# Kernel optimization log

Measured on AMD Instinct MI355X. Metric: run time of the kernel, lower is better.

## Reference

```python
import jax, jax.numpy as jnp
import numpy as np

D_MODEL = 1024
N_HEADS = 16
D_K = D_MODEL // N_HEADS
BATCH = 4
SEQ = 2048


def setup_inputs() -> dict:
    key = jax.random.key(0)
    ks = jax.random.split(key, 12)
    s = 1.0 / np.sqrt(D_MODEL)
    inp = {
        "query": jax.random.normal(ks[0], (BATCH, SEQ, D_MODEL), jnp.float32),
        "key": jax.random.normal(ks[1], (BATCH, SEQ, D_MODEL), jnp.float32),
        "value": jax.random.normal(ks[2], (BATCH, SEQ, D_MODEL), jnp.float32),
        # causal mask: True = masked (ignored), broadcastable over batch/heads
        "mask": jnp.triu(jnp.ones((SEQ, SEQ), bool), k=1)[None, None, :, :],
        "w_q": jax.random.normal(ks[3], (D_MODEL, D_MODEL), jnp.float32) * s,
        "b_q": jax.random.normal(ks[4], (D_MODEL,), jnp.float32) * s,
        "w_k": jax.random.normal(ks[5], (D_MODEL, D_MODEL), jnp.float32) * s,
        "b_k": jax.random.normal(ks[6], (D_MODEL,), jnp.float32) * s,
        "w_v": jax.random.normal(ks[7], (D_MODEL, D_MODEL), jnp.float32) * s,
        "b_v": jax.random.normal(ks[8], (D_MODEL,), jnp.float32) * s,
        "w_o": jax.random.normal(ks[9], (D_MODEL, D_MODEL), jnp.float32) * s,
        "b_o": jax.random.normal(ks[10], (D_MODEL,), jnp.float32) * s,
    }
    return inp


def _split_heads(x):
    # (B, S, D) -> (B, H, S, d_k)
    b, s, _ = x.shape
    return x.reshape(b, s, N_HEADS, D_K).transpose(0, 2, 1, 3)


def reference(query, key, value, mask, w_q, b_q, w_k, b_k, w_v, b_v, w_o, b_o):
    # torch Linear: y = x @ W.T + b
    q = _split_heads(query @ w_q.T + b_q)
    k = _split_heads(key @ w_k.T + b_k)
    v = _split_heads(value @ w_v.T + b_v)
    scale = 1.0 / jnp.sqrt(jnp.asarray(D_K, q.dtype))
    scores = jnp.einsum("bhqd,bhkd->bhqk", q, k) * scale
    scores = jnp.where(mask, jnp.asarray(-jnp.inf, scores.dtype), scores)
    weights = jax.nn.softmax(scores, axis=-1)  # dropout p=0.0 (eval)
    attn = jnp.einsum("bhqk,bhkd->bhqd", weights, v)
    b = attn.shape[0]
    attn = attn.transpose(0, 2, 1, 3).reshape(b, -1, D_MODEL)
    return attn @ w_o.T + b_o
```

## Files before the change

kernel.cpp:

```cpp
#include <hip/hip_runtime.h>

#define S_LEN 2048
#define DMODEL 1024
#define H_CNT 16
#define DK 64
#define BATCH 4

typedef __attribute__((ext_vector_type(8))) short short8;
typedef __attribute__((ext_vector_type(4))) float f32x4;
typedef __attribute__((ext_vector_type(16))) float f32x16;

static __device__ __forceinline__ short f2bf(float f) {
  union { float f; unsigned u; } x; x.f = f;
  unsigned r = x.u + 0x7fffu + ((x.u >> 16) & 1u);
  return (short)(r >> 16);
}

static __device__ __forceinline__ unsigned cvt_pk_bf16(float lo, float hi) {
  unsigned r;
  asm("v_cvt_pk_bf16_f32 %0, %1, %2" : "=v"(r) : "v"(lo), "v"(hi));
  return r;
}

static __device__ __forceinline__ void gl_lds16(const short* g, short* l) {
  __builtin_amdgcn_global_load_lds((const __attribute__((address_space(1))) void*)g,
                                   (__attribute__((address_space(3))) void*)l, 16, 0, 0);
}

__global__ __launch_bounds__(256) void cast_kernel(const float* __restrict__ src,
                                                   short* __restrict__ dst, int n8) {
  int i = blockIdx.x * 256 + threadIdx.x;
  if (i >= n8) return;
  const float4* s4 = (const float4*)src;
  float4 a = s4[2 * i], b = s4[2 * i + 1];
  short8 o;
  o[0] = f2bf(a.x); o[1] = f2bf(a.y); o[2] = f2bf(a.z); o[3] = f2bf(a.w);
  o[4] = f2bf(b.x); o[5] = f2bf(b.y); o[6] = f2bf(b.z); o[7] = f2bf(b.w);
  ((short8*)dst)[i] = o;
}

template <int MODE>
__global__ __launch_bounds__(256) void gemm_bt(const short* __restrict__ A,
                                               const short* __restrict__ B,
                                               const float* __restrict__ bias,
                                               void* __restrict__ Cout,
                                               int M, int N, int K, float scl) {
  __shared__ short Sab[(128 + 64) * 32];
  const int tid = threadIdx.x;
  const int lane = tid & 63, wid = tid >> 6;
  const int lin = blockIdx.x;
  const int w = (lin & 7) * 128 + (lin >> 3);
  int bx, by;
  if (MODE == 1) { bx = w >> 3; by = w & 7; }
  else           { bx = w & 15; by = w >> 4; }
  const int m0 = by * 128, n0 = bx * 64;
  const int wr = wid * 32;
  const int lrow = lane & 15, lk8 = (lane >> 4) * 8;

  const int l4 = lane >> 2, lc = (lane & 3) * 8;
  const short* gsrc[3];
  short* ldst[3];
#pragma unroll
  for (int i = 0; i < 3; i++) {
    int c = wid * 3 + i;
    ldst[i] = &Sab[c * 512];
    if (c < 8) gsrc[i] = &A[(size_t)(m0 + c * 16 + l4) * K + lc];
    else       gsrc[i] = &B[(size_t)(n0 + (c - 8) * 16 + l4) * K + lc];
  }

  f32x4 acc[2][4] = {};

  for (int k0 = 0; k0 < K; k0 += 32) {
#pragma unroll
    for (int i = 0; i < 3; i++) gl_lds16(gsrc[i] + k0, ldst[i]);
    __syncthreads();
    short8 af[2], bfr[4];
#pragma unroll
    for (int m = 0; m < 2; m++) af[m] = *(const short8*)(&Sab[(wr + m * 16 + lrow) * 32 + lk8]);
#pragma unroll
    for (int n = 0; n < 4; n++) bfr[n] = *(const short8*)(&Sab[(128 + n * 16 + lrow) * 32 + lk8]);
#pragma unroll
    for (int m = 0; m < 2; m++)
#pragma unroll
      for (int n = 0; n < 4; n++)
        acc[m][n] = __builtin_amdgcn_mfma_f32_16x16x32_bf16(af[m], bfr[n], acc[m][n], 0, 0, 0);
    __syncthreads();
  }

  const int g4 = (lane >> 4) * 4;
#pragma unroll
  for (int n = 0; n < 4; n++) {
    const int col = n0 + n * 16 + lrow;
#pragma unroll
    for (int m = 0; m < 2; m++) {
#pragma unroll
      for (int i = 0; i < 4; i++) {
        const int row = m0 + wr + m * 16 + g4 + i;
        float val = acc[m][n][i];
        if (MODE == 0) {
          val = (val + bias[col]) * scl;
          int b = row >> 11, s2 = row & 2047, h = col >> 6, d = col & 63;
          ((short*)Cout)[((size_t)(b * H_CNT + h) * S_LEN + s2) * DK + d] = f2bf(val);
        } else if (MODE == 1) {
          val = val + bias[row];
          int h = row >> 6, d = row & 63, b = col >> 11, s2 = col & 2047;
          ((short*)Cout)[((size_t)(b * H_CNT + h) * DK + d) * S_LEN + s2] = f2bf(val);
        } else {
          val = val + bias[col];
          ((float*)Cout)[(size_t)row * N + col] = val;
        }
      }
    }
  }
}

__global__ __launch_bounds__(256, 4) void attn2_kernel(const short* __restrict__ Q,
                                                       const short* __restrict__ Kc,
                                                       const short* __restrict__ Vt,
                                                       short* __restrict__ Oout) {
  const int bh = blockIdx.y;
  const int j = blockIdx.x;
  const int wid = threadIdx.x >> 6, lane = threadIdx.x & 63;
  const int qt = (wid == 0) ? j : (wid == 1) ? (31 - j) : (wid == 2) ? (32 + j) : (63 - j);
  const int q0 = qt * 32;
  const int ql = lane & 31, hl = lane >> 5;

  const short* Qb = Q + (size_t)bh * S_LEN * DK;
  const short* Kb = Kc + (size_t)bh * S_LEN * DK;
  const short* Vb = Vt + (size_t)bh * DK * S_LEN;

  short8 qf[4];
#pragma unroll
  for (int kk = 0; kk < 4; kk++)
    qf[kk] = *(const short8*)(&Qb[(q0 + ql) * DK + kk * 16 + hl * 8]);

  f32x16 oacc[2] = {};
  float mr = -1e30f, lr = 0.f;

  const int ntiles = qt + 1;
  for (int t = 0; t < ntiles; t++) {
    const int kv0 = t * 32;
    f32x16 st = {};
#pragma unroll
    for (int kk = 0; kk < 4; kk++) {
      short8 kf = *(const short8*)(&Kb[(kv0 + ql) * DK + kk * 16 + hl * 8]);
      st = __builtin_amdgcn_mfma_f32_32x32x16_bf16(kf, qf[kk], st, 0, 0, 0);
    }
    short8 vf[2][2];
#pragma unroll
    for (int td = 0; td < 2; td++)
#pragma unroll
      for (int kk = 0; kk < 2; kk++)
        vf[td][kk] = *(const short8*)(&Vb[(size_t)(td * 32 + ql) * S_LEN + kv0 + kk * 16 + hl * 8]);

    float p[16];
#pragma unroll
    for (int r = 0; r < 16; r++) p[r] = st[r];
    if (t == ntiles - 1) {
#pragma unroll
      for (int r = 0; r < 16; r++) {
        int kvr = (r & 3) + 8 * (r >> 2) + 4 * hl;
        if (kvr > ql) p[r] = -1e30f;
      }
    }
    float pm = p[0];
#pragma unroll
    for (int r = 1; r < 16; r++) pm = fmaxf(pm, p[r]);
    pm = fmaxf(pm, __shfl_xor(pm, 32, 64));
    if (!__all(pm <= mr + 8.f)) {
      float mnew = fmaxf(mr, pm);
      float al = __builtin_amdgcn_exp2f(mr - mnew);
      lr *= al;
#pragma unroll
      for (int td = 0; td < 2; td++)
#pragma unroll
        for (int r = 0; r < 16; r++) oacc[td][r] *= al;
      mr = mnew;
    }
    float rs = 0.f;
#pragma unroll
    for (int r = 0; r < 16; r++) {
      p[r] = __builtin_amdgcn_exp2f(p[r] - mr);
      rs += p[r];
    }
    rs += __shfl_xor(rs, 32, 64);
    lr += rs;

    unsigned wpk[8];
#pragma unroll
    for (int tt = 0; tt < 8; tt++) wpk[tt] = cvt_pk_bf16(p[2 * tt], p[2 * tt + 1]);
    union { short8 s; unsigned u[4]; } bf0, bf1;
    {
      unsigned xa = __shfl_xor((int)wpk[2], 32, 64), xb = __shfl_xor((int)wpk[0], 32, 64);
      bf0.u[0] = hl ? xa : wpk[0];
      bf0.u[2] = hl ? wpk[2] : xb;
    }
    {
      unsigned xa = __shfl_xor((int)wpk[3], 32, 64), xb = __shfl_xor((int)wpk[1], 32, 64);
      bf0.u[1] = hl ? xa : wpk[1];
      bf0.u[3] = hl ? wpk[3] : xb;
    }
    {
      unsigned xa = __shfl_xor((int)wpk[6], 32, 64), xb = __shfl_xor((int)wpk[4], 32, 64);
      bf1.u[0] = hl ? xa : wpk[4];
      bf1.u[2] = hl ? wpk[6] : xb;
    }
    {
      unsigned xa = __shfl_xor((int)wpk[7], 32, 64), xb = __shfl_xor((int)wpk[5], 32, 64);
      bf1.u[1] = hl ? xa : wpk[5];
      bf1.u[3] = hl ? wpk[7] : xb;
    }

#pragma unroll
    for (int td = 0; td < 2; td++) {
      oacc[td] = __builtin_amdgcn_mfma_f32_32x32x16_bf16(vf[td][0], bf0.s, oacc[td], 0, 0, 0);
      oacc[td] = __builtin_amdgcn_mfma_f32_32x32x16_bf16(vf[td][1], bf1.s, oacc[td], 0, 0, 0);
    }
  }

  const float inv = __builtin_amdgcn_rcpf(lr);
  const int b = bh >> 4, h = bh & 15;
  unsigned* ob = (unsigned*)Oout + ((size_t)b * S_LEN + q0 + ql) * (DMODEL / 2) + h * (DK / 2);
#pragma unroll
  for (int td = 0; td < 2; td++)
#pragma unroll
    for (int tt = 0; tt < 8; tt++) {
      unsigned pkv = cvt_pk_bf16(oacc[td][2 * tt] * inv, oacc[td][2 * tt + 1] * inv);
      ob[td * 16 + (tt & 1) + 4 * (tt >> 1) + 2 * hl] = pkv;
    }
}

extern "C" void kernel_launch(void* const* d_in, const int* in_sizes, int n_in,
                              void* d_out, int out_size, void* d_ws, size_t ws_size,
                              hipStream_t stream) {
  (void)in_sizes; (void)n_in; (void)out_size; (void)ws_size;
  const float* query = (const float*)d_in[0];
  const float* key_i = (const float*)d_in[1];
  const float* value = (const float*)d_in[2];
  const float* w_q = (const float*)d_in[4];
  const float* b_q = (const float*)d_in[5];
  const float* w_k = (const float*)d_in[6];
  const float* b_k = (const float*)d_in[7];
  const float* w_v = (const float*)d_in[8];
  const float* b_v = (const float*)d_in[9];
  const float* w_o = (const float*)d_in[10];
  const float* b_o = (const float*)d_in[11];

  const size_t XE = (size_t)BATCH * S_LEN * DMODEL;
  const size_t WE = (size_t)DMODEL * DMODEL;

  short* xq = (short*)d_ws;
  short* xk = xq + XE;
  short* xv = xk + XE;
  short* wq = xv + XE;
  short* wk = wq + WE;
  short* wv = wk + WE;
  short* wo = wv + WE;
  short* qb = wo + WE;
  short* kb = qb + XE;
  short* vtb = kb + XE;
  short* attnb = xq;

  const int M = BATCH * S_LEN;

  int n8x = (int)(XE / 8), n8w = (int)(WE / 8);
  cast_kernel<<<dim3((n8x + 255) / 256), 256, 0, stream>>>(query, xq, n8x);
  cast_kernel<<<dim3((n8x + 255) / 256), 256, 0, stream>>>(key_i, xk, n8x);
  cast_kernel<<<dim3((n8x + 255) / 256), 256, 0, stream>>>(value, xv, n8x);
  cast_kernel<<<dim3((n8w + 255) / 256), 256, 0, stream>>>(w_q, wq, n8w);
  cast_kernel<<<dim3((n8w + 255) / 256), 256, 0, stream>>>(w_k, wk, n8w);
  cast_kernel<<<dim3((n8w + 255) / 256), 256, 0, stream>>>(w_v, wv, n8w);
  cast_kernel<<<dim3((n8w + 255) / 256), 256, 0, stream>>>(w_o, wo, n8w);

  const float qscale = 0.125f * 1.44269504088896f;

  gemm_bt<0><<<1024, 256, 0, stream>>>(xq, wq, b_q, qb, M, DMODEL, DMODEL, qscale);
  gemm_bt<0><<<1024, 256, 0, stream>>>(xk, wk, b_k, kb, M, DMODEL, DMODEL, 1.f);
  gemm_bt<1><<<1024, 256, 0, stream>>>(wv, xv, b_v, vtb, DMODEL, M, DMODEL, 1.f);

  attn2_kernel<<<dim3(16, BATCH * H_CNT), 256, 0, stream>>>(qb, kb, vtb, attnb);

  gemm_bt<2><<<1024, 256, 0, stream>>>(attnb, wo, b_o, d_out, M, DMODEL, DMODEL, 1.f);
}
```

Measured before the change: 278.0 us.

## Pair causal q-tiles per wave and prefetch next K tile in attention

Each wave now handles two query tiles (p and 63-p) one after the other, so every wave gets the same total causal work. Blocks shrink from 256 to 128 threads, so each block has half as many waves. The K fragments for the next KV tile are loaded into registers before the current tile's MFMA and softmax work, so global load latency can overlap with compute. This raises register pressure and halves the number of concurrent waves per block. The launch bound changes from (256,4) to (128,2), which may reduce occupancy.

```diff
diff --git a/kernel.cpp b/kernel.cpp
--- a/kernel.cpp
+++ b/kernel.cpp
@@ -114,120 +114,135 @@
   }
 }
 
-__global__ __launch_bounds__(256, 4) void attn2_kernel(const short* __restrict__ Q,
+__global__ __launch_bounds__(128, 2) void attn2_kernel(const short* __restrict__ Q,
                                                        const short* __restrict__ Kc,
                                                        const short* __restrict__ Vt,
                                                        short* __restrict__ Oout) {
   const int bh = blockIdx.y;
-  const int j = blockIdx.x;
   const int wid = threadIdx.x >> 6, lane = threadIdx.x & 63;
-  const int qt = (wid == 0) ? j : (wid == 1) ? (31 - j) : (wid == 2) ? (32 + j) : (63 - j);
-  const int q0 = qt * 32;
+  const int p = blockIdx.x * 2 + wid;
   const int ql = lane & 31, hl = lane >> 5;
 
   const short* Qb = Q + (size_t)bh * S_LEN * DK;
   const short* Kb = Kc + (size_t)bh * S_LEN * DK;
   const short* Vb = Vt + (size_t)bh * DK * S_LEN;
-
-  short8 qf[4];
-#pragma unroll
-  for (int kk = 0; kk < 4; kk++)
-    qf[kk] = *(const short8*)(&Qb[(q0 + ql) * DK + kk * 16 + hl * 8]);
-
-  f32x16 oacc[2] = {};
-  float mr = -1e30f, lr = 0.f;
-
-  const int ntiles = qt + 1;
-  for (int t = 0; t < ntiles; t++) {
-    const int kv0 = t * 32;
-    f32x16 st = {};
-#pragma unroll
-    for (int kk = 0; kk < 4; kk++) {
-      short8 kf = *(const short8*)(&Kb[(kv0 + ql) * DK + kk * 16 + hl * 8]);
-      st = __builtin_amdgcn_mfma_f32_32x32x16_bf16(kf, qf[kk], st, 0, 0, 0);
+  const int b = bh >> 4, h = bh & 15;
+
+  for (int phase = 0; phase < 2; ++phase) {
+    const int qt = phase ? (63 - p) : p;
+    const int q0 = qt * 32;
+
+    short8 qf[4];
+#pragma unroll
+    for (int kk = 0; kk < 4; kk++)
+      qf[kk] = *(const short8*)(&Qb[(q0 + ql) * DK + kk * 16 + hl * 8]);
+
+    f32x16 oacc[2] = {};
+    float mr = -1e30f, lr = 0.f;
+
+    short8 kf[4];
+#pragma unroll
+    for (int kk = 0; kk < 4; kk++)
+      kf[kk] = *(const short8*)(&Kb[ql * DK + kk * 16 + hl * 8]);
+
+    const int ntiles = qt + 1;
+    for (int t = 0; t < ntiles; t++) {
+      const int kv0 = t * 32;
+      const int kvn = (t + 1 < ntiles) ? kv0 + 32 : kv0;
+      short8 kfn[4];
+#pragma unroll
+      for (int kk = 0; kk < 4; kk++)
+        kfn[kk] = *(const short8*)(&Kb[(kvn + ql) * DK + kk * 16 + hl * 8]);
+      short8 vf[2][2];
+#pragma unroll
+      for (int td = 0; td < 2; td++)
+#pragma unroll
+        for (int kk = 0; kk < 2; kk++)
+          vf[td][kk] = *(const short8*)(&Vb[(size_t)(td * 32 + ql) * S_LEN + kv0 + kk * 16 + hl * 8]);
+
+      f32x16 st = {};
+#pragma unroll
+      for (int kk = 0; kk < 4; kk++)
+        st = __builtin_amdgcn_mfma_f32_32x32x16_bf16(kf[kk], qf[kk], st, 0, 0, 0);
+
+      float pv[16];
+#pragma unroll
+      for (int r = 0; r < 16; r++) pv[r] = st[r];
+      if (t == ntiles - 1) {
+#pragma unroll
+        for (int r = 0; r < 16; r++) {
+          int kvr = (r & 3) + 8 * (r >> 2) + 4 * hl;
+          if (kvr > ql) pv[r] = -1e30f;
+        }
+      }
+      float pm = pv[0];
+#pragma unroll
+      for (int r = 1; r < 16; r++) pm = fmaxf(pm, pv[r]);
+      pm = fmaxf(pm, __shfl_xor(pm, 32, 64));
+      if (!__all(pm <= mr + 8.f)) {
+        float mnew = fmaxf(mr, pm);
+        float al = __builtin_amdgcn_exp2f(mr - mnew);
+        lr *= al;
+#pragma unroll
+        for (int td = 0; td < 2; td++)
+#pragma unroll
+          for (int r = 0; r < 16; r++) oacc[td][r] *= al;
+        mr = mnew;
+      }
+      float rs = 0.f;
+#pragma unroll
+      for (int r = 0; r < 16; r++) {
+        pv[r] = __builtin_amdgcn_exp2f(pv[r] - mr);
+        rs += pv[r];
+      }
+      rs += __shfl_xor(rs, 32, 64);
+      lr += rs;
+
+      unsigned wpk[8];
+#pragma unroll
+      for (int tt = 0; tt < 8; tt++) wpk[tt] = cvt_pk_bf16(pv[2 * tt], pv[2 * tt + 1]);
+      union { short8 s; unsigned u[4]; } bf0, bf1;
+      {
+        unsigned xa = __shfl_xor((int)wpk[2], 32, 64), xb = __shfl_xor((int)wpk[0], 32, 64);
+        bf0.u[0] = hl ? xa : wpk[0];
+        bf0.u[2] = hl ? wpk[2] : xb;
+      }
+      {
+        unsigned xa = __shfl_xor((int)wpk[3], 32, 64), xb = __shfl_xor((int)wpk[1], 32, 64);
+        bf0.u[1] = hl ? xa : wpk[1];
+        bf0.u[3] = hl ? wpk[3] : xb;
+      }
+      {
+        unsigned xa = __shfl_xor((int)wpk[6], 32, 64), xb = __shfl_xor((int)wpk[4], 32, 64);
+        bf1.u[0] = hl ? xa : wpk[4];
+        bf1.u[2] = hl ? wpk[6] : xb;
+      }
+      {
+        unsigned xa = __shfl_xor((int)wpk[7], 32, 64), xb = __shfl_xor((int)wpk[5], 32, 64);
+        bf1.u[1] = hl ? xa : wpk[5];
+        bf1.u[3] = hl ? wpk[7] : xb;
+      }
+
+#pragma unroll
+      for (int td = 0; td < 2; td++) {
+        oacc[td] = __builtin_amdgcn_mfma_f32_32x32x16_bf16(vf[td][0], bf0.s, oacc[td], 0, 0, 0);
+        oacc[td] = __builtin_amdgcn_mfma_f32_32x32x16_bf16(vf[td][1], bf1.s, oacc[td], 0, 0, 0);
+      }
+
+#pragma unroll
+      for (int kk = 0; kk < 4; kk++) kf[kk] = kfn[kk];
     }
-    short8 vf[2][2];
+
+    const float inv = __builtin_amdgcn_rcpf(lr);
+    unsigned* ob = (unsigned*)Oout + ((size_t)b * S_LEN + q0 + ql) * (DMODEL / 2) + h * (DK / 2);
 #pragma unroll
     for (int td = 0; td < 2; td++)
 #pragma unroll
-      for (int kk = 0; kk < 2; kk++)
-        vf[td][kk] = *(const short8*)(&Vb[(size_t)(td * 32 + ql) * S_LEN + kv0 + kk * 16 + hl * 8]);
-
-    float p[16];
-#pragma unroll
-    for (int r = 0; r < 16; r++) p[r] = st[r];
-    if (t == ntiles - 1) {
-#pragma unroll
-      for (int r = 0; r < 16; r++) {
-        int kvr = (r & 3) + 8 * (r >> 2) + 4 * hl;
-        if (kvr > ql) p[r] = -1e30f;
-      }
-    }
-    float pm = p[0];
-#pragma unroll
-    for (int r = 1; r < 16; r++) pm = fmaxf(pm, p[r]);
-    pm = fmaxf(pm, __shfl_xor(pm, 32, 64));
-    if (!__all(pm <= mr + 8.f)) {
-      float mnew = fmaxf(mr, pm);
-      float al = __builtin_amdgcn_exp2f(mr - mnew);
-      lr *= al;
-#pragma unroll
-      for (int td = 0; td < 2; td++)
-#pragma unroll
-        for (int r = 0; r < 16; r++) oacc[td][r] *= al;
-      mr = mnew;
-    }
-    float rs = 0.f;
-#pragma unroll
-    for (int r = 0; r < 16; r++) {
-      p[r] = __builtin_amdgcn_exp2f(p[r] - mr);
-      rs += p[r];
-    }
-    rs += __shfl_xor(rs, 32, 64);
-    lr += rs;
-
-    unsigned wpk[8];
-#pragma unroll
-    for (int tt = 0; tt < 8; tt++) wpk[tt] = cvt_pk_bf16(p[2 * tt], p[2 * tt + 1]);
-    union { short8 s; unsigned u[4]; } bf0, bf1;
-    {
-      unsigned xa = __shfl_xor((int)wpk[2], 32, 64), xb = __shfl_xor((int)wpk[0], 32, 64);
-      bf0.u[0] = hl ? xa : wpk[0];
-      bf0.u[2] = hl ? wpk[2] : xb;
-    }
-    {
-      unsigned xa = __shfl_xor((int)wpk[3], 32, 64), xb = __shfl_xor((int)wpk[1], 32, 64);
-      bf0.u[1] = hl ? xa : wpk[1];
-      bf0.u[3] = hl ? wpk[3] : xb;
-    }
-    {
-      unsigned xa = __shfl_xor((int)wpk[6], 32, 64), xb = __shfl_xor((int)wpk[4], 32, 64);
-      bf1.u[0] = hl ? xa : wpk[4];
-      bf1.u[2] = hl ? wpk[6] : xb;
-    }
-    {
-      unsigned xa = __shfl_xor((int)wpk[7], 32, 64), xb = __shfl_xor((int)wpk[5], 32, 64);
-      bf1.u[1] = hl ? xa : wpk[5];
-      bf1.u[3] = hl ? wpk[7] : xb;
-    }
-
-#pragma unroll
-    for (int td = 0; td < 2; td++) {
-      oacc[td] = __builtin_amdgcn_mfma_f32_32x32x16_bf16(vf[td][0], bf0.s, oacc[td], 0, 0, 0);
-      oacc[td] = __builtin_amdgcn_mfma_f32_32x32x16_bf16(vf[td][1], bf1.s, oacc[td], 0, 0, 0);
-    }
-  }
-
-  const float inv = __builtin_amdgcn_rcpf(lr);
-  const int b = bh >> 4, h = bh & 15;
-  unsigned* ob = (unsigned*)Oout + ((size_t)b * S_LEN + q0 + ql) * (DMODEL / 2) + h * (DK / 2);
-#pragma unroll
-  for (int td = 0; td < 2; td++)
-#pragma unroll
-    for (int tt = 0; tt < 8; tt++) {
-      unsigned pkv = cvt_pk_bf16(oacc[td][2 * tt] * inv, oacc[td][2 * tt + 1] * inv);
-      ob[td * 16 + (tt & 1) + 4 * (tt >> 1) + 2 * hl] = pkv;
-    }
+      for (int tt = 0; tt < 8; tt++) {
+        unsigned pkv = cvt_pk_bf16(oacc[td][2 * tt] * inv, oacc[td][2 * tt + 1] * inv);
+        ob[td * 16 + (tt & 1) + 4 * (tt >> 1) + 2 * hl] = pkv;
+      }
+  }
 }
 
 extern "C" void kernel_launch(void* const* d_in, const int* in_sizes, int n_in,
@@ -278,7 +293,7 @@
   gemm_bt<0><<<1024, 256, 0, stream>>>(xk, wk, b_k, kb, M, DMODEL, DMODEL, 1.f);
   gemm_bt<1><<<1024, 256, 0, stream>>>(wv, xv, b_v, vtb, DMODEL, M, DMODEL, 1.f);
 
-  attn2_kernel<<<dim3(16, BATCH * H_CNT), 256, 0, stream>>>(qb, kb, vtb, attnb);
+  attn2_kernel<<<dim3(16, BATCH * H_CNT), 128, 0, stream>>>(qb, kb, vtb, attnb);
 
   gemm_bt<2><<<1024, 256, 0, stream>>>(attnb, wo, b_o, d_out, M, DMODEL, DMODEL, 1.f);
 }
```

Measured after the change: 278.9 us. No clear change (+0.3%).

## Process 64-key tiles per iteration in attention with unconditional rescale

Applied to the files above, without the earlier changes.

The attention inner loop now handles two 32-key chunks per iteration. It issues both chunks' K/V loads up front and computes two score tiles before one softmax update, which halves the number of max/rescale/shuffle rounds and exposes more memory-level parallelism. The lazy rescale threshold is replaced by an unconditional rescale, and the exponent is clamped at zero for safety. Occupancy hint drops from 4 to 2 blocks per CU to allow more registers, which risks lower latency hiding and some wasted masked work on the last tile.

```diff
diff --git a/kernel.cpp b/kernel.cpp
--- a/kernel.cpp
+++ b/kernel.cpp
@@ -114,7 +114,7 @@
   }
 }
 
-__global__ __launch_bounds__(256, 4) void attn2_kernel(const short* __restrict__ Q,
+__global__ __launch_bounds__(256, 2) void attn2_kernel(const short* __restrict__ Q,
                                                        const short* __restrict__ Kc,
                                                        const short* __restrict__ Vt,
                                                        short* __restrict__ Oout) {
@@ -137,84 +137,107 @@
   f32x16 oacc[2] = {};
   float mr = -1e30f, lr = 0.f;
 
-  const int ntiles = qt + 1;
-  for (int t = 0; t < ntiles; t++) {
-    const int kv0 = t * 32;
-    f32x16 st = {};
-#pragma unroll
-    for (int kk = 0; kk < 4; kk++) {
-      short8 kf = *(const short8*)(&Kb[(kv0 + ql) * DK + kk * 16 + hl * 8]);
-      st = __builtin_amdgcn_mfma_f32_32x32x16_bf16(kf, qf[kk], st, 0, 0, 0);
-    }
-    short8 vf[2][2];
+  const int nt = qt / 2 + 1;
+  for (int t = 0; t < nt; t++) {
+    const int kv0 = t * 64;
+
+    short8 kf[2][4];
+#pragma unroll
+    for (int c = 0; c < 2; c++)
+#pragma unroll
+      for (int kk = 0; kk < 4; kk++)
+        kf[c][kk] = *(const short8*)(&Kb[(kv0 + 32 * c + ql) * DK + kk * 16 + hl * 8]);
+    short8 vf[2][2][2];
 #pragma unroll
     for (int td = 0; td < 2; td++)
 #pragma unroll
-      for (int kk = 0; kk < 2; kk++)
-        vf[td][kk] = *(const short8*)(&Vb[(size_t)(td * 32 + ql) * S_LEN + kv0 + kk * 16 + hl * 8]);
-
-    float p[16];
-#pragma unroll
-    for (int r = 0; r < 16; r++) p[r] = st[r];
-    if (t == ntiles - 1) {
-#pragma unroll
-      for (int r = 0; r < 16; r++) {
-        int kvr = (r & 3) + 8 * (r >> 2) + 4 * hl;
-        if (kvr > ql) p[r] = -1e30f;
-      }
-    }
+      for (int c = 0; c < 2; c++)
+#pragma unroll
+        for (int k2 = 0; k2 < 2; k2++)
+          vf[td][c][k2] =
+              *(const short8*)(&Vb[(size_t)(td * 32 + ql) * S_LEN + kv0 + 32 * c + k2 * 16 + hl * 8]);
+
+    f32x16 st0 = {}, st1 = {};
+#pragma unroll
+    for (int kk = 0; kk < 4; kk++)
+      st0 = __builtin_amdgcn_mfma_f32_32x32x16_bf16(kf[0][kk], qf[kk], st0, 0, 0, 0);
+#pragma unroll
+    for (int kk = 0; kk < 4; kk++)
+      st1 = __builtin_amdgcn_mfma_f32_32x32x16_bf16(kf[1][kk], qf[kk], st1, 0, 0, 0);
+
+    float p[32];
+#pragma unroll
+    for (int r = 0; r < 16; r++) { p[r] = st0[r]; p[16 + r] = st1[r]; }
+
+#pragma unroll
+    for (int c = 0; c < 2; c++) {
+      const int base = kv0 + 32 * c;
+      if (base == q0) {
+#pragma unroll
+        for (int r = 0; r < 16; r++) {
+          int kvr = (r & 3) + 8 * (r >> 2) + 4 * hl;
+          if (kvr > ql) p[16 * c + r] = -1e30f;
+        }
+      } else if (base > q0) {
+#pragma unroll
+        for (int r = 0; r < 16; r++) p[16 * c + r] = -1e30f;
+      }
+    }
+
     float pm = p[0];
 #pragma unroll
-    for (int r = 1; r < 16; r++) pm = fmaxf(pm, p[r]);
+    for (int r = 1; r < 32; r++) pm = fmaxf(pm, p[r]);
     pm = fmaxf(pm, __shfl_xor(pm, 32, 64));
-    if (!__all(pm <= mr + 8.f)) {
-      float mnew = fmaxf(mr, pm);
-      float al = __builtin_amdgcn_exp2f(mr - mnew);
-      lr *= al;
-#pragma unroll
-      for (int td = 0; td < 2; td++)
-#pragma unroll
-        for (int r = 0; r < 16; r++) oacc[td][r] *= al;
-      mr = mnew;
-    }
+    const float mnew = fmaxf(mr, pm);
+    const float al = __builtin_amdgcn_exp2f(mr - mnew);
+    mr = mnew;
+    lr *= al;
+#pragma unroll
+    for (int td = 0; td < 2; td++)
+#pragma unroll
+      for (int r = 0; r < 16; r++) oacc[td][r] *= al;
+
     float rs = 0.f;
 #pragma unroll
-    for (int r = 0; r < 16; r++) {
-      p[r] = __builtin_amdgcn_exp2f(p[r] - mr);
+    for (int r = 0; r < 32; r++) {
+      p[r] = __builtin_amdgcn_exp2f(fminf(p[r] - mr, 0.f));
       rs += p[r];
     }
     rs += __shfl_xor(rs, 32, 64);
     lr += rs;
 
-    unsigned wpk[8];
-#pragma unroll
-    for (int tt = 0; tt < 8; tt++) wpk[tt] = cvt_pk_bf16(p[2 * tt], p[2 * tt + 1]);
-    union { short8 s; unsigned u[4]; } bf0, bf1;
-    {
-      unsigned xa = __shfl_xor((int)wpk[2], 32, 64), xb = __shfl_xor((int)wpk[0], 32, 64);
-      bf0.u[0] = hl ? xa : wpk[0];
-      bf0.u[2] = hl ? wpk[2] : xb;
-    }
-    {
-      unsigned xa = __shfl_xor((int)wpk[3], 32, 64), xb = __shfl_xor((int)wpk[1], 32, 64);
-      bf0.u[1] = hl ? xa : wpk[1];
-      bf0.u[3] = hl ? wpk[3] : xb;
-    }
-    {
-      unsigned xa = __shfl_xor((int)wpk[6], 32, 64), xb = __shfl_xor((int)wpk[4], 32, 64);
-      bf1.u[0] = hl ? xa : wpk[4];
-      bf1.u[2] = hl ? wpk[6] : xb;
-    }
-    {
-      unsigned xa = __shfl_xor((int)wpk[7], 32, 64), xb = __shfl_xor((int)wpk[5], 32, 64);
-      bf1.u[1] = hl ? xa : wpk[5];
-      bf1.u[3] = hl ? wpk[7] : xb;
-    }
-
-#pragma unroll
-    for (int td = 0; td < 2; td++) {
-      oacc[td] = __builtin_amdgcn_mfma_f32_32x32x16_bf16(vf[td][0], bf0.s, oacc[td], 0, 0, 0);
-      oacc[td] = __builtin_amdgcn_mfma_f32_32x32x16_bf16(vf[td][1], bf1.s, oacc[td], 0, 0, 0);
+#pragma unroll
+    for (int c = 0; c < 2; c++) {
+      unsigned wpk[8];
+#pragma unroll
+      for (int tt = 0; tt < 8; tt++)
+        wpk[tt] = cvt_pk_bf16(p[16 * c + 2 * tt], p[16 * c + 2 * tt + 1]);
+      union { short8 s; unsigned u[4]; } bf0, bf1;
+      {
+        unsigned xa = __shfl_xor((int)wpk[2], 32, 64), xb = __shfl_xor((int)wpk[0], 32, 64);
+        bf0.u[0] = hl ? xa : wpk[0];
+        bf0.u[2] = hl ? wpk[2] : xb;
+      }
+      {
+        unsigned xa = __shfl_xor((int)wpk[3], 32, 64), xb = __shfl_xor((int)wpk[1], 32, 64);
+        bf0.u[1] = hl ? xa : wpk[1];
+        bf0.u[3] = hl ? wpk[3] : xb;
+      }
+      {
+        unsigned xa = __shfl_xor((int)wpk[6], 32, 64), xb = __shfl_xor((int)wpk[4], 32, 64);
+        bf1.u[0] = hl ? xa : wpk[4];
+        bf1.u[2] = hl ? wpk[6] : xb;
+      }
+      {
+        unsigned xa = __shfl_xor((int)wpk[7], 32, 64), xb = __shfl_xor((int)wpk[5], 32, 64);
+        bf1.u[1] = hl ? xa : wpk[5];
+        bf1.u[3] = hl ? wpk[7] : xb;
+      }
+#pragma unroll
+      for (int td = 0; td < 2; td++) {
+        oacc[td] = __builtin_amdgcn_mfma_f32_32x32x16_bf16(vf[td][c][0], bf0.s, oacc[td], 0, 0, 0);
+        oacc[td] = __builtin_amdgcn_mfma_f32_32x32x16_bf16(vf[td][c][1], bf1.s, oacc[td], 0, 0, 0);
+      }
     }
   }
 
```

Result: slower. 291.3 us (+4.8%).
